# Performance work log

Measured on AMD Instinct MI355X. Metric: run time of the kernel, lower is better.

Reference implementation:

```python
import jax, jax.numpy as jnp
import numpy as np

jax.config.update("jax_enable_x64", True)  # torch code casts to double for the logdet

B, N = 64, 512
MIN_LEN = 384  # variable sentence lengths to exercise padding path


def _matrix_tree_logZ(s_arc, mask):
    """log partition of non-projective trees via Kirchhoff's Matrix-Tree theorem.

    s_arc: [B, n, n] float32 scores of (dependent i, head j) pairs.
    mask:  [B, n] bool, column 0 is the root pseudo-word (False on input).
    """
    n = s_arc.shape[-1]
    m = mask.at[:, 0].set(True)                      # index_fill(1, 0, 1)
    chart = m[:, :, None] & m[:, None, :]            # [B, n, n]
    s = jnp.where(chart, s_arc, -jnp.inf)            # masked_fill(~chart, -inf)
    A = jnp.exp(s).astype(jnp.float64)               # exp(-inf) = 0 on padding
    d = A.sum(-1)                                    # D diagonal: row sums [B, n]
    eye = jnp.eye(n, dtype=A.dtype)
    L_full = d[:, :, None] * eye - A                 # D - A (Laplacian)
    # rows of padding tokens are identity rows (masked_scatter_ onto eye)
    L = jnp.where(m[:, :, None], L_full, eye[None])
    # logdet of the minor removing root row/col
    _, logabsdet = jnp.linalg.slogdet(L[:, 1:, 1:])
    return logabsdet.sum().astype(jnp.float32)


def setup_inputs() -> dict:
    key = jax.random.key(0)
    k1, k2, k3 = jax.random.split(key, 3)
    scores = jax.random.normal(k1, (B, N, N), dtype=jnp.float32)
    lens = jax.random.randint(k2, (B,), MIN_LEN, N)
    pos = jnp.arange(N)
    # first column False (root pseudo-word), True for real tokens < length
    mask = (pos[None, :] < lens[:, None]) & (pos[None, :] > 0)
    target = jax.random.randint(k3, (B, N), 0, N)    # gold head indices
    return {"scores": scores, "mask": mask, "target": target}


def reference(scores, mask, target):
    # forward(scores, mask, target, mbr=True, partial=False)
    logZ, marginals = jax.value_and_grad(_matrix_tree_logZ)(scores, mask)
    gold = jnp.take_along_axis(scores, target[..., None], axis=-1).squeeze(-1)  # [B, N]
    gold_score = jnp.where(mask, gold, 0.0).sum()    # scores[mask].sum()
    loss = (logZ - gold_score) / mask.sum()
    return loss, marginals
```

## Files before the change

kernel.cpp:

```cpp
#include <hip/hip_runtime.h>
#include <math.h>

#define BATCH 64
#define NN 512
#define MS 511
#define LDM 512
#define MSTRIDE ((size_t)MS*LDM)
#define OSTRIDE ((size_t)NN*NN)
#define PB 64
#define YW(r,c) (((r)<<5) + ((((c) + ((((r)>>3)&7)<<2))) & 31))

__global__ void k_convert(const void* __restrict__ mask_raw,
                          const void* __restrict__ tgt_raw,
                          int* __restrict__ cmask, int* __restrict__ ctgt) {
  int b = blockIdx.x;
  const unsigned char* mb = (const unsigned char*)mask_raw;
  const int* mw = (const int*)mask_raw;
  const int* tw = (const int*)tgt_raw;
  bool m_bytes = (mb[1] | mb[2] | mb[3]) != 0;
  bool m_64 = false;
  if (!m_bytes) {
    int acc = 0;
    for (int j = 1; j < 32; j += 2) acc |= mw[j];
    m_64 = (acc == 0);
  }
  int tacc = 0;
  for (int j = 1; j < 32; j += 2) tacc |= tw[j];
  bool t_64 = (tacc == 0);
  for (int i = threadIdx.x; i < NN; i += blockDim.x) {
    size_t idx = (size_t)b * NN + i;
    int mv;
    if (m_bytes) mv = mb[idx] != 0;
    else if (m_64) mv = mw[2 * idx] != 0;
    else mv = mw[idx] != 0;
    cmask[idx] = mv;
    ctgt[idx] = t_64 ? tw[2 * idx] : tw[idx];
  }
}

__global__ void k_build_M(const float* __restrict__ scores,
                          const int* __restrict__ mask,
                          float* __restrict__ M) {
  int b = blockIdx.y;
  int ip = blockIdx.x;
  int i = ip + 1;
  const int* mrow = mask + (size_t)b * NN;
  float* Mrow = M + (size_t)b * MSTRIDE + (size_t)ip * LDM;
  int tid = threadIdx.x;
  if (!mrow[i]) {
    for (int jp = tid; jp < MS; jp += 256)
      Mrow[jp] = (jp == ip) ? 1.0f : 0.0f;
    if (tid == 0) Mrow[MS] = 0.0f;
    return;
  }
  const float* srow = scores + ((size_t)b * NN + i) * NN;
  double part = 0.0;
  for (int j = tid; j < NN; j += 256) {
    bool mj = (j == 0) || (mrow[j] != 0);
    float e = mj ? expf(srow[j]) : 0.0f;
    part += (double)e;
    if (j >= 1) Mrow[j - 1] = -e;
  }
  __shared__ double red[256];
  red[tid] = part;
  __syncthreads();
  for (int s = 128; s > 0; s >>= 1) {
    if (tid < s) red[tid] += red[tid + s];
    __syncthreads();
  }
  if (tid == (i & 255)) Mrow[ip] += (float)red[0];
  if (tid == 0) Mrow[MS] = 0.0f;
}

__global__ __launch_bounds__(512) void k_panel64(float* __restrict__ M, int kb,
                                                 double* __restrict__ ld2) {
  int b = blockIdx.x;
  float* Mb = M + (size_t)b * MSTRIDE;
  int tid = threadIdx.x;
  __shared__ float A[64 * 65];
  __shared__ float XU[64 * 66];
  __shared__ float XL[64 * 66];
  __shared__ double lg[64];

  for (int idx = tid; idx < 64 * 64; idx += 512) {
    int r = idx >> 6, c = idx & 63;
    int gr = kb + r, gc = kb + c;
    A[r * 65 + c] = (gr < MS && gc < MS) ? Mb[(size_t)gr * LDM + gc]
                                         : ((r == c) ? 1.0f : 0.0f);
  }
  __syncthreads();

  int rr = tid >> 3, sub = tid & 7;
  for (int j = 0; j < 63; ++j) {
    if (rr > j) {
      float piv = A[j * 65 + j];
      float l = A[rr * 65 + j] / piv;
      if (sub == 0) A[rr * 65 + j] = l;
      for (int c = j + 1 + sub; c < 64; c += 8)
        A[rr * 65 + c] -= l * A[j * 65 + c];
    }
    __syncthreads();
  }
  if (tid < 64) lg[tid] = log(fabs((double)A[tid * 65 + tid]));
  __syncthreads();
  if (tid == 0) {
    double a = 0.0;
    for (int j = 0; j < 64; ++j) a += lg[j];
    ld2[(kb >> 6) * BATCH + b] = a;
  }

  {
    int c = rr;
    if (sub == 0) XU[c * 66 + c] = 1.0f / A[c * 65 + c];
    for (int r2 = c - 1; r2 >= 0; --r2) {
      float s = 0.0f;
      for (int k = r2 + 1 + sub; k <= c; k += 8)
        s += A[r2 * 65 + k] * XU[c * 66 + k];
      s += __shfl_xor(s, 1, 8);
      s += __shfl_xor(s, 2, 8);
      s += __shfl_xor(s, 4, 8);
      if (sub == 0) XU[c * 66 + r2] = -s / A[r2 * 65 + r2];
    }
  }
  {
    int c = rr;
    if (sub == 0) XL[c * 66 + c] = 1.0f;
    for (int r2 = c + 1; r2 < 64; ++r2) {
      float s = 0.0f;
      for (int k = c + sub; k < r2; k += 8)
        s += A[r2 * 65 + k] * XL[c * 66 + k];
      s += __shfl_xor(s, 1, 8);
      s += __shfl_xor(s, 2, 8);
      s += __shfl_xor(s, 4, 8);
      if (sub == 0) XL[c * 66 + r2] = -s;
    }
  }
  __syncthreads();
  for (int idx = tid; idx < 4096; idx += 512) {
    int r = idx >> 6, c = idx & 63;
    int gr = kb + r, gc = kb + c;
    if (gr < MS && gc < MS)
      Mb[(size_t)gr * LDM + gc] = (r > c) ? XL[c * 66 + r] : XU[c * 66 + r];
  }
}

__global__ __launch_bounds__(256) void k_trsm(float* __restrict__ M, int kb) {
  int b = blockIdx.z;
  int t = blockIdx.x;
  int side = blockIdx.y;
  float* Mb = M + (size_t)b * MSTRIDE;
  __shared__ float Fs[64 * 65];
  __shared__ float As[64 * 65];
  int tid = threadIdx.x;
  int off = kb + 64 + t * 64;
  for (int idx = tid; idx < 4096; idx += 256) {
    int r = idx >> 6, c = idx & 63;
    int gr = kb + r, gc = kb + c;
    float v;
    if (gr < MS && gc < MS) {
      float d = Mb[(size_t)gr * LDM + gc];
      if (side == 0) v = (r > c) ? d : (r == c ? 1.0f : 0.0f);
      else           v = (r <= c) ? d : 0.0f;
    } else {
      v = (r == c) ? 1.0f : 0.0f;
    }
    Fs[r * 65 + c] = v;
  }
  for (int idx = tid; idx < 4096; idx += 256) {
    int r = idx >> 6, c = idx & 63;
    int gr, gc;
    if (side == 0) { gr = kb + r; gc = off + c; }
    else           { gr = off + r; gc = kb + c; }
    As[r * 65 + c] = (gr < MS && gc < MS) ? Mb[(size_t)gr * LDM + gc] : 0.0f;
  }
  __syncthreads();
  int tx = tid & 15, ty = tid >> 4;
  float acc[4][4];
#pragma unroll
  for (int i = 0; i < 4; ++i)
#pragma unroll
    for (int j = 0; j < 4; ++j) acc[i][j] = 0.0f;
  if (side == 0) {
#pragma unroll 4
    for (int k = 0; k < 64; ++k) {
      float av[4], bv[4];
#pragma unroll
      for (int i = 0; i < 4; ++i) av[i] = Fs[(ty * 4 + i) * 65 + k];
#pragma unroll
      for (int j = 0; j < 4; ++j) bv[j] = As[k * 65 + tx * 4 + j];
#pragma unroll
      for (int i = 0; i < 4; ++i)
#pragma unroll
        for (int j = 0; j < 4; ++j) acc[i][j] = fmaf(av[i], bv[j], acc[i][j]);
    }
  } else {
#pragma unroll 4
    for (int k = 0; k < 64; ++k) {
      float av[4], bv[4];
#pragma unroll
      for (int i = 0; i < 4; ++i) av[i] = As[(ty * 4 + i) * 65 + k];
#pragma unroll
      for (int j = 0; j < 4; ++j) bv[j] = Fs[k * 65 + tx * 4 + j];
#pragma unroll
      for (int i = 0; i < 4; ++i)
#pragma unroll
        for (int j = 0; j < 4; ++j) acc[i][j] = fmaf(av[i], bv[j], acc[i][j]);
    }
  }
  if (side == 0) {
    int gc = off + tx * 4;
    if (gc < MS) {
#pragma unroll
      for (int i = 0; i < 4; ++i) {
        int gr = kb + ty * 4 + i;
        *(float4*)&Mb[(size_t)gr * LDM + gc] =
            make_float4(acc[i][0], acc[i][1], acc[i][2], acc[i][3]);
      }
    }
  } else {
#pragma unroll
    for (int i = 0; i < 4; ++i) {
      int gr = off + ty * 4 + i;
      if (gr < MS)
        *(float4*)&Mb[(size_t)gr * LDM + kb + tx * 4] =
            make_float4(acc[i][0], acc[i][1], acc[i][2], acc[i][3]);
    }
  }
}

__global__ __launch_bounds__(256) void k_update(float* __restrict__ M, int kb) {
  int b = blockIdx.z;
  float* Mb = M + (size_t)b * MSTRIDE;
  int row0 = kb + PB + blockIdx.x * 128;
  int col0 = kb + PB + blockIdx.y * 128;
  __shared__ __align__(16) float As[128 * 68];
  __shared__ __align__(16) float Bs[64 * 132];
  int tid = threadIdx.x;
  for (int idx = tid; idx < 2048; idx += 256) {
    int r = idx >> 4, q = (idx & 15) * 4;
    int gr = row0 + r;
    float4 v = make_float4(0.f, 0.f, 0.f, 0.f);
    if (gr < MS) v = *(const float4*)&Mb[(size_t)gr * LDM + kb + q];
    *(float4*)&As[r * 68 + q] = v;
  }
  for (int idx = tid; idx < 2048; idx += 256) {
    int r = idx >> 5, q = (idx & 31) * 4;
    int gc = col0 + q;
    float4 v = make_float4(0.f, 0.f, 0.f, 0.f);
    if (gc < MS)
      v = *(const float4*)&Mb[(size_t)(kb + r) * LDM + gc];
    *(float4*)&Bs[r * 132 + q] = v;
  }
  __syncthreads();
  int tx = tid & 15, ty = tid >> 4;
  int gc0 = col0 + tx * 4, gc1 = gc0 + 64;
  bool c0v = gc0 < MS, c1v = gc1 < MS;
  float4 acc[8][2];
#pragma unroll
  for (int i = 0; i < 8; ++i) {
    int gr = row0 + ty + 16 * i;
    bool rv = gr < MS;
    acc[i][0] = (rv && c0v) ? *(const float4*)&Mb[(size_t)gr * LDM + gc0]
                            : make_float4(0.f, 0.f, 0.f, 0.f);
    acc[i][1] = (rv && c1v) ? *(const float4*)&Mb[(size_t)gr * LDM + gc1]
                            : make_float4(0.f, 0.f, 0.f, 0.f);
  }
#pragma unroll 2
  for (int k = 0; k < 64; ++k) {
    float4 b0 = *(const float4*)&Bs[k * 132 + tx * 4];
    float4 b1 = *(const float4*)&Bs[k * 132 + tx * 4 + 64];
    float av[8];
#pragma unroll
    for (int i = 0; i < 8; ++i) av[i] = As[(ty + 16 * i) * 68 + k];
#pragma unroll
    for (int i = 0; i < 8; ++i) {
      float a = av[i];
      acc[i][0].x = fmaf(-a, b0.x, acc[i][0].x);
      acc[i][0].y = fmaf(-a, b0.y, acc[i][0].y);
      acc[i][0].z = fmaf(-a, b0.z, acc[i][0].z);
      acc[i][0].w = fmaf(-a, b0.w, acc[i][0].w);
      acc[i][1].x = fmaf(-a, b1.x, acc[i][1].x);
      acc[i][1].y = fmaf(-a, b1.y, acc[i][1].y);
      acc[i][1].z = fmaf(-a, b1.z, acc[i][1].z);
      acc[i][1].w = fmaf(-a, b1.w, acc[i][1].w);
    }
  }
#pragma unroll
  for (int i = 0; i < 8; ++i) {
    int gr = row0 + ty + 16 * i;
    if (gr < MS) {
      if (c0v) *(float4*)&Mb[(size_t)gr * LDM + gc0] = acc[i][0];
      if (c1v) *(float4*)&Mb[(size_t)gr * LDM + gc1] = acc[i][1];
    }
  }
}

__device__ __forceinline__ void diag_pass(const float* __restrict__ Mb,
                                          float* __restrict__ Yt,
                                          int jb, int tid, int UPPER) {
  int drg = tid >> 3, dcg = tid & 7;
  int dr = jb + drg;
  bool vr = dr < MS;
  const float* Pr = Mb + (size_t)dr * LDM + jb;
  float4 da = make_float4(0.f, 0.f, 0.f, 0.f);
#pragma unroll 4
  for (int q = 0; q < 16; ++q) {
    float4 t = vr ? *(const float4*)&Pr[4 * q] : make_float4(0.f, 0.f, 0.f, 0.f);
#pragma unroll
    for (int m = 0; m < 4; ++m) {
      int cc = 4 * q + m;
      float tm = (m == 0) ? t.x : ((m == 1) ? t.y : ((m == 2) ? t.z : t.w));
      float a;
      if (UPPER) a = (drg <= cc) ? tm : 0.0f;
      else       a = (drg > cc) ? tm : ((drg == cc) ? 1.0f : 0.0f);
      float4 bv = *(const float4*)&Yt[YW(jb + cc, 4 * dcg)];
      da.x = fmaf(a, bv.x, da.x); da.y = fmaf(a, bv.y, da.y);
      da.z = fmaf(a, bv.z, da.z); da.w = fmaf(a, bv.w, da.w);
    }
  }
  __syncthreads();
  *(float4*)&Yt[YW(jb + drg, 4 * dcg)] = da;
  __syncthreads();
}

__device__ __forceinline__ void offdiag_pass(const float* __restrict__ Mb,
                                             float* __restrict__ Yt,
                                             int jb, int rowBase, int nr,
                                             int tid, int cg, int rg) {
  if (nr <= 0) return;
  int row0 = rowBase + 8 * rg;
  int nv = nr - 8 * rg;
  if (nv <= 0) return;
  nv = nv > 8 ? 8 : nv;
  float4 a0[8];
#pragma unroll
  for (int i = 0; i < 8; ++i)
    a0[i] = (i < nv) ? *(const float4*)&Yt[YW(row0 + i, 4 * cg)]
                     : make_float4(0.f, 0.f, 0.f, 0.f);
  const float* Ar = Mb + (size_t)row0 * LDM + jb;
#pragma unroll 2
  for (int kh = 0; kh < 16; ++kh) {
    float4 pA[8];
#pragma unroll
    for (int i = 0; i < 8; ++i)
      pA[i] = (i < nv) ? *(const float4*)&Ar[(size_t)i * LDM + 4 * kh]
                       : make_float4(0.f, 0.f, 0.f, 0.f);
    __builtin_amdgcn_s_setprio(1);
#pragma unroll
    for (int k = 0; k < 4; ++k) {
      float4 bv = *(const float4*)&Yt[YW(jb + 4 * kh + k, 4 * cg)];
#define AK(i) ((k == 0) ? pA[i].x : ((k == 1) ? pA[i].y : ((k == 2) ? pA[i].z : pA[i].w)))
#define RF(i) { \
      float av_ = AK(i); \
      a0[i].x = fmaf(-av_, bv.x, a0[i].x); a0[i].y = fmaf(-av_, bv.y, a0[i].y); \
      a0[i].z = fmaf(-av_, bv.z, a0[i].z); a0[i].w = fmaf(-av_, bv.w, a0[i].w); }
      RF(0) RF(1) RF(2) RF(3) RF(4) RF(5) RF(6) RF(7)
#undef RF
#undef AK
    }
    __builtin_amdgcn_s_setprio(0);
  }
#pragma unroll
  for (int i = 0; i < 8; ++i) {
    if (i < nv)
      *(float4*)&Yt[YW(row0 + i, 4 * cg)] = a0[i];
  }
}

__global__ __launch_bounds__(512, 4) void k_solve(const float* __restrict__ M,
                                                  const float* __restrict__ scores,
                                                  const int* __restrict__ mask,
                                                  float* __restrict__ out1) {
  int id = blockIdx.x;
  int xcd = id & 7, k7 = id >> 3;
  int b = xcd + ((k7 >> 4) << 3);
  int cb = k7 & 15;
  const float* Mb = M + (size_t)b * MSTRIDE;
  int tid = threadIdx.x;
  int c0 = cb * 32, fb = c0 & ~63;
  __shared__ __align__(16) float Yt[512 * 32];
  int cg = tid & 7, rg = tid >> 3;

  for (int idx = tid; idx < 4096; idx += 512)
    ((float4*)Yt)[idx] = make_float4(0.f, 0.f, 0.f, 0.f);
  __syncthreads();
  {
    int coff = c0 - fb;
    int r2 = tid >> 3, q4 = (tid & 7) << 2;
    int gr = fb + r2;
    int c_ = coff + q4;
    float e0, e1, e2, e3;
    if (gr < MS) {
      float4 d = *(const float4*)&Mb[(size_t)gr * LDM + fb + c_];
      e0 = (r2 > c_) ? d.x : ((r2 == c_) ? 1.f : 0.f);
      e1 = (r2 > c_ + 1) ? d.y : ((r2 == c_ + 1) ? 1.f : 0.f);
      e2 = (r2 > c_ + 2) ? d.z : ((r2 == c_ + 2) ? 1.f : 0.f);
      e3 = (r2 > c_ + 3) ? d.w : ((r2 == c_ + 3) ? 1.f : 0.f);
    } else {
      e0 = (r2 == c_) ? 1.f : 0.f;
      e1 = (r2 == c_ + 1) ? 1.f : 0.f;
      e2 = (r2 == c_ + 2) ? 1.f : 0.f;
      e3 = (r2 == c_ + 3) ? 1.f : 0.f;
    }
    *(float4*)&Yt[YW(gr, q4)] = make_float4(e0, e1, e2, e3);
  }
  __syncthreads();

  for (int jb = fb; jb < MS; jb += 64) {
    if (jb > fb) {
      __syncthreads();
      diag_pass(Mb, Yt, jb, tid, 0);
    }
    offdiag_pass(Mb, Yt, jb, jb + 64, MS - (jb + 64), tid, cg, rg);
  }
  for (int jb = 448; jb >= 0; jb -= 64) {
    __syncthreads();
    diag_pass(Mb, Yt, jb, tid, 1);
    offdiag_pass(Mb, Yt, jb, 0, jb, tid, cg, rg);
  }
  __syncthreads();

  const int* mrow = mask + (size_t)b * NN;
  const float* sb = scores + (size_t)b * NN * NN;
  float* ob = out1 + (size_t)b * OSTRIDE;
  for (int c = 0; c < 32; ++c) {
    int cgl = c0 + c;
    if (cgl >= MS) break;
    int i = cgl + 1;
    float* orow = ob + (size_t)i * NN;
    if (mrow[i] == 0) {
      orow[tid] = 0.0f;
    } else {
      float kd = Yt[YW(i - 1, c)];
      int k = tid;
      bool mk = (k == 0) || (mrow[k] != 0);
      float v = 0.0f;
      if (mk) {
        float s2 = (k >= 1) ? Yt[YW(k - 1, c)] : 0.0f;
        v = expf(sb[(size_t)i * NN + k]) * (kd - s2);
      }
      orow[k] = v;
    }
  }
  if (cb == 0) ob[tid] = 0.0f;
}

__global__ void k_gold(const float* __restrict__ scores,
                       const int* __restrict__ mask,
                       const int* __restrict__ target,
                       double* __restrict__ goldb, int* __restrict__ cntb) {
  int b = blockIdx.x;
  const int* mrow = mask + (size_t)b * NN;
  const int* trow = target + (size_t)b * NN;
  double g = 0.0;
  int c = 0;
  for (int i = threadIdx.x; i < NN; i += blockDim.x) {
    if (mrow[i] != 0) {
      g += (double)scores[((size_t)b * NN + i) * NN + trow[i]];
      c++;
    }
  }
  __shared__ double gs[256];
  __shared__ int cs[256];
  gs[threadIdx.x] = g;
  cs[threadIdx.x] = c;
  __syncthreads();
  for (int s = 128; s > 0; s >>= 1) {
    if (threadIdx.x < s) {
      gs[threadIdx.x] += gs[threadIdx.x + s];
      cs[threadIdx.x] += cs[threadIdx.x + s];
    }
    __syncthreads();
  }
  if (threadIdx.x == 0) { goldb[b] = gs[0]; cntb[b] = cs[0]; }
}

__global__ void k_final(const double* __restrict__ ld2,
                        const double* __restrict__ goldb,
                        const int* __restrict__ cntb, float* __restrict__ out) {
  int tid = threadIdx.x;
  double lz = 0.0, g = 0.0;
  double cnt = 0.0;
  for (int s = tid; s < 8 * BATCH; s += 256) lz += ld2[s];
  if (tid < BATCH) { g = goldb[tid]; cnt = (double)cntb[tid]; }
  __shared__ double r0[256], r1[256], r2[256];
  r0[tid] = lz; r1[tid] = g; r2[tid] = cnt;
  __syncthreads();
  for (int s = 128; s > 0; s >>= 1) {
    if (tid < s) { r0[tid] += r0[tid + s]; r1[tid] += r1[tid + s]; r2[tid] += r2[tid + s]; }
    __syncthreads();
  }
  if (tid == 0) out[0] = (float)((r0[0] - r1[0]) / r2[0]);
}

extern "C" void kernel_launch(void* const* d_in, const int* in_sizes, int n_in,
                              void* d_out, int out_size, void* d_ws, size_t ws_size,
                              hipStream_t stream) {
  const float* scores = (const float*)d_in[0];
  const void* mask_raw = d_in[1];
  const void* tgt_raw = d_in[2];
  float* out = (float*)d_out;
  float* out1 = out + 1;

  float* Mbuf = (float*)d_ws;
  size_t moff = (MSTRIDE * BATCH * sizeof(float) + 255) & ~(size_t)255;
  double* ld2 = (double*)((char*)d_ws + moff);
  double* goldb = ld2 + 8 * BATCH;
  int* cntb = (int*)(goldb + BATCH);
  int* cmask = cntb + BATCH;
  int* ctgt = cmask + BATCH * NN;

  k_convert<<<BATCH, 256, 0, stream>>>(mask_raw, tgt_raw, cmask, ctgt);
  k_build_M<<<dim3(MS, BATCH), 256, 0, stream>>>(scores, cmask, Mbuf);

  for (int kb = 0; kb < MS; kb += PB) {
    k_panel64<<<BATCH, 512, 0, stream>>>(Mbuf, kb, ld2);
    int rem2 = MS - kb - PB;
    if (rem2 > 0) {
      int nt64 = (rem2 + 63) / 64;
      k_trsm<<<dim3(nt64, 2, BATCH), 256, 0, stream>>>(Mbuf, kb);
      int nt128 = (rem2 + 127) / 128;
      k_update<<<dim3(nt128, nt128, BATCH), 256, 0, stream>>>(Mbuf, kb);
    }
  }

  k_solve<<<dim3(1024), 512, 0, stream>>>(Mbuf, scores, cmask, out1);
  k_gold<<<BATCH, 256, 0, stream>>>(scores, cmask, ctgt, goldb, cntb);
  k_final<<<1, 256, 0, stream>>>(ld2, goldb, cntb, out);
}
```

Before: 1.159 ms.

## Fuse next diagonal panel factorization into trailing update kernel

Removes the separate per-step panel kernel launch after the first step. The (0,0) block of the trailing update now also factors the next 64x64 diagonal block, records its log-determinant, and writes the inverted triangular factors back. This cuts seven launches and their serialization gaps. In exchange, one block per batch does serial LU and triangular-inverse work with only 256 threads and many syncthreads, which may lengthen the update kernel's critical path. The panel also now uses float LU without the original kernel's pivoting or precision logic, which is unknown.

```diff
diff --git a/kernel.cpp b/kernel.cpp
--- a/kernel.cpp
+++ b/kernel.cpp
@@ -228,13 +228,16 @@
   }
 }
 
-__global__ __launch_bounds__(256) void k_update(float* __restrict__ M, int kb) {
+__global__ __launch_bounds__(256) void k_update_panel(float* __restrict__ M, int kb,
+                                                      double* __restrict__ ld2) {
   int b = blockIdx.z;
   float* Mb = M + (size_t)b * MSTRIDE;
   int row0 = kb + PB + blockIdx.x * 128;
   int col0 = kb + PB + blockIdx.y * 128;
-  __shared__ __align__(16) float As[128 * 68];
-  __shared__ __align__(16) float Bs[64 * 132];
+  __shared__ __align__(16) float smem[128 * 68 + 64 * 132];
+  __shared__ double lg[64];
+  float* As = smem;
+  float* Bs = smem + 128 * 68;
   int tid = threadIdx.x;
   for (int idx = tid; idx < 2048; idx += 256) {
     int r = idx >> 4, q = (idx & 15) * 4;
@@ -291,6 +294,70 @@
     if (gr < MS) {
       if (c0v) *(float4*)&Mb[(size_t)gr * LDM + gc0] = acc[i][0];
       if (c1v) *(float4*)&Mb[(size_t)gr * LDM + gc1] = acc[i][1];
+    }
+  }
+
+  if (blockIdx.x == 0 && blockIdx.y == 0) {
+    int kbn = kb + PB;
+    float* A2 = smem;
+    float* XU = smem + 4160;
+    float* XL = smem + 4160 + 4224;
+    __syncthreads();
+    for (int idx = tid; idx < 4096; idx += 256) {
+      int r = idx >> 6, c = idx & 63;
+      int gr = kbn + r, gc = kbn + c;
+      A2[r * 65 + c] = (gr < MS && gc < MS) ? Mb[(size_t)gr * LDM + gc]
+                                            : ((r == c) ? 1.0f : 0.0f);
+    }
+    __syncthreads();
+    int rr = tid >> 2, sub = tid & 3;
+    for (int j = 0; j < 63; ++j) {
+      if (rr > j) {
+        float piv = A2[j * 65 + j];
+        float l = A2[rr * 65 + j] / piv;
+        if (sub == 0) A2[rr * 65 + j] = l;
+        for (int c = j + 1 + sub; c < 64; c += 4)
+          A2[rr * 65 + c] -= l * A2[j * 65 + c];
+      }
+      __syncthreads();
+    }
+    if (tid < 64) lg[tid] = log(fabs((double)A2[tid * 65 + tid]));
+    __syncthreads();
+    if (tid == 0) {
+      double a = 0.0;
+      for (int j = 0; j < 64; ++j) a += lg[j];
+      ld2[(kbn >> 6) * BATCH + b] = a;
+    }
+    {
+      int c = rr;
+      if (sub == 0) XU[c * 66 + c] = 1.0f / A2[c * 65 + c];
+      for (int r2 = c - 1; r2 >= 0; --r2) {
+        float s = 0.0f;
+        for (int k = r2 + 1 + sub; k <= c; k += 4)
+          s += A2[r2 * 65 + k] * XU[c * 66 + k];
+        s += __shfl_xor(s, 1, 4);
+        s += __shfl_xor(s, 2, 4);
+        if (sub == 0) XU[c * 66 + r2] = -s / A2[r2 * 65 + r2];
+      }
+    }
+    {
+      int c = rr;
+      if (sub == 0) XL[c * 66 + c] = 1.0f;
+      for (int r2 = c + 1; r2 < 64; ++r2) {
+        float s = 0.0f;
+        for (int k = c + sub; k < r2; k += 4)
+          s += A2[r2 * 65 + k] * XL[c * 66 + k];
+        s += __shfl_xor(s, 1, 4);
+        s += __shfl_xor(s, 2, 4);
+        if (sub == 0) XL[c * 66 + r2] = -s;
+      }
+    }
+    __syncthreads();
+    for (int idx = tid; idx < 4096; idx += 256) {
+      int r = idx >> 6, c = idx & 63;
+      int gr = kbn + r, gc = kbn + c;
+      if (gr < MS && gc < MS)
+        Mb[(size_t)gr * LDM + gc] = (r > c) ? XL[c * 66 + r] : XU[c * 66 + r];
     }
   }
 }
@@ -513,15 +580,13 @@
   k_convert<<<BATCH, 256, 0, stream>>>(mask_raw, tgt_raw, cmask, ctgt);
   k_build_M<<<dim3(MS, BATCH), 256, 0, stream>>>(scores, cmask, Mbuf);
 
-  for (int kb = 0; kb < MS; kb += PB) {
-    k_panel64<<<BATCH, 512, 0, stream>>>(Mbuf, kb, ld2);
+  k_panel64<<<BATCH, 512, 0, stream>>>(Mbuf, 0, ld2);
+  for (int kb = 0; kb + PB < MS; kb += PB) {
     int rem2 = MS - kb - PB;
-    if (rem2 > 0) {
-      int nt64 = (rem2 + 63) / 64;
-      k_trsm<<<dim3(nt64, 2, BATCH), 256, 0, stream>>>(Mbuf, kb);
-      int nt128 = (rem2 + 127) / 128;
-      k_update<<<dim3(nt128, nt128, BATCH), 256, 0, stream>>>(Mbuf, kb);
-    }
+    int nt64 = (rem2 + 63) / 64;
+    k_trsm<<<dim3(nt64, 2, BATCH), 256, 0, stream>>>(Mbuf, kb);
+    int nt128 = (rem2 + 127) / 128;
+    k_update_panel<<<dim3(nt128, nt128, BATCH), 256, 0, stream>>>(Mbuf, kb, ld2);
   }
 
   k_solve<<<dim3(1024), 512, 0, stream>>>(Mbuf, scores, cmask, out1);
```

Result: slower. 1.370 ms (+18.3%).
